# Performance work log

Hardware: AMD Instinct MI355X
Metric: run time of the kernel (lower is better)

The kernel has to match this reference:

```python
import jax, jax.numpy as jnp
import numpy as np

MIN_BW = 0.1
MAX_BW = 10.0
BW_FACTOR = 1.0
SAMPLE = 512  # min(512, B) with B >= 512


def _pairwise_dist_sq(a, b):
    # ||a_i - b_j||^2 via GEMM: [N, M], avoids [N, M, D] intermediate
    a2 = jnp.sum(a * a, axis=-1)[:, None]
    b2 = jnp.sum(b * b, axis=-1)[None, :]
    d = a2 + b2 - 2.0 * (a @ b.T)
    return jnp.maximum(d, 0.0)


def _bandwidth(x, y):
    # torch: median heuristic on first SAMPLE rows, under no_grad
    xs = jax.lax.stop_gradient(x[:SAMPLE])
    ys = jax.lax.stop_gradient(y[:SAMPLE])
    dist_sq = _pairwise_dist_sq(xs, ys)
    bw_sq = jnp.median(dist_sq.reshape(-1))
    bw = jnp.sqrt(bw_sq / 2.0) * BW_FACTOR
    return jnp.clip(bw, MIN_BW, MAX_BW)


def setup_inputs() -> dict:
    key = jax.random.key(0)
    kx, ksx, ky, ksy = jax.random.split(key, 4)
    B, D = 4096, 512
    return {
        "x": jax.random.normal(kx, (B, D), dtype=jnp.float32),
        "score_x": jax.random.normal(ksx, (B, D), dtype=jnp.float32),
        "y": jax.random.normal(ky, (B, D), dtype=jnp.float32),
        "score_y": jax.random.normal(ksy, (B, D), dtype=jnp.float32),
    }


def reference(x, score_x, y, score_y):
    D = x.shape[-1]
    h = _bandwidth(x, y)
    h2 = h * h

    dist_sq = _pairwise_dist_sq(x, y)                      # [B, B]
    k = jnp.exp(-dist_sq / (2.0 * h2))                     # [B, B]

    # term1[i,j] = k[i,j] * <score_x_i, score_y_j>
    term1 = k * (score_x @ score_y.T)

    # term2[i,j] = <x_i - y_j, score_y_j> * k[i,j] / h^2
    term2 = ((x @ score_y.T) - jnp.sum(y * score_y, axis=-1)[None, :]) * k / h2

    # term3[i,j] = ||x_i - y_j||^2 * k / h^4 - k * D / h^2
    term3 = dist_sq * k / (h2 * h2) - k * (D / h2)

    return term1 + term2 + term3
```

## Files before the change

### kernel.cpp

```cpp
#include <hip/hip_runtime.h>
#include <hip/hip_bf16.h>

typedef __attribute__((ext_vector_type(8))) short bf16x8;
typedef __attribute__((ext_vector_type(4))) float f32x4;

#define B_N 4096
#define DIM 512
#define HBINS 8192

#define OFF_PARAMS 0
#define OFF_X2     256
#define OFF_Y2     16640
#define OFF_YSY    33024
#define OFF_HIST   49408
#define OFF_TILES  98304
#define MAT_ELEMS  2097152
#define WS_NEED    (OFF_TILES + (size_t)4 * MAT_ELEMS * 2)

static __device__ __forceinline__ unsigned short f2bf_rne(float f) {
    unsigned int u = __float_as_uint(f);
    u += 0x7FFFu + ((u >> 16) & 1u);
    return (unsigned short)(u >> 16);
}
static __device__ __forceinline__ float bf2f(unsigned short h) {
    return __uint_as_float(((unsigned int)h) << 16);
}

static __device__ __forceinline__ int swz(int r, int k) {
    return r * 32 + ((((k >> 3) ^ ((r >> 1) & 3))) << 3) + (k & 7);
}


__global__ __launch_bounds__(256) void k_preAll(
    const float* __restrict__ X, const float* __restrict__ Y,
    const float* __restrict__ SY, unsigned short* __restrict__ tiles,
    float* __restrict__ x2, float* __restrict__ y2, float* __restrict__ ysy,
    unsigned int* __restrict__ hist) {
    __shared__ __align__(16) unsigned short sAB[4096];
    __shared__ unsigned int hloc[HBINS];
    __shared__ float rn[128];

    int b = blockIdx.x, t = threadIdx.x;

    if (b < 512) {
        int side = b >> 8;
        int tile = (b & 255) >> 3;
        int ky = b & 7;
        unsigned short* base0 = tiles + (size_t)side * 2 * MAT_ELEMS;
        unsigned short* base1 = base0 + MAT_ELEMS;
#pragma unroll
        for (int kt2 = 0; kt2 < 2; ++kt2) {
            int kt = ky * 2 + kt2;
            unsigned short* d0 = base0 + (size_t)(tile * 16 + kt) * 4096;
            unsigned short* d1 = base1 + (size_t)(tile * 16 + kt) * 4096;
#pragma unroll
            for (int c = 0; c < 2; ++c) {
                int v = c * 256 + t;
                int r = (v >> 6) * 16 + (v & 15);
                int k = ((v >> 4) & 3) << 3;
                const float* gp = (side ? Y : X) + (size_t)(tile * 128 + r) * DIM + kt * 32 + k;
                float4 p0 = *(const float4*)gp;
                float4 p1 = *(const float4*)(gp + 4);
                float pv[8] = {p0.x, p0.y, p0.z, p0.w, p1.x, p1.y, p1.z, p1.w};
                float s1 = 0.f, s2 = 0.f;
                bf16x8 h0;
                if (side) {
                    const float* gq = SY + (size_t)(tile * 128 + r) * DIM + kt * 32 + k;
                    float4 q0 = *(const float4*)gq;
                    float4 q1 = *(const float4*)(gq + 4);
                    float qv[8] = {q0.x, q0.y, q0.z, q0.w, q1.x, q1.y, q1.z, q1.w};
                    bf16x8 h1;
#pragma unroll
                    for (int j = 0; j < 8; ++j) {
                        s1 += pv[j] * pv[j];
                        s2 += pv[j] * qv[j];
                        h0[j] = (short)f2bf_rne(pv[j]);
                        h1[j] = (short)f2bf_rne(qv[j]);
                    }
                    *(bf16x8*)&d1[v * 8] = h1;
                } else {
#pragma unroll
                    for (int j = 0; j < 8; ++j) {
                        s1 += pv[j] * pv[j];
                        h0[j] = (short)f2bf_rne(pv[j]);
                    }
                }
                *(bf16x8*)&d0[v * 8] = h0;
                s1 += __shfl_xor(s1, 16); s1 += __shfl_xor(s1, 32);
                if (side) { s2 += __shfl_xor(s2, 16); s2 += __shfl_xor(s2, 32); }
                if ((t & 48) == 0) {
                    int row = tile * 128 + r;
                    if (side == 0) {
                        atomicAdd(&x2[row], s1);
                    } else {
                        atomicAdd(&y2[row], s1);
                        atomicAdd(&ysy[row], s2);
                    }
                }
            }
        }
    } else {
        unsigned short* sA = &sAB[0];
        unsigned short* sB = &sAB[2048];
        float* x2s = &rn[0];
        float* y2s = &rn[64];
        int hb = b - 512;
        int bi = hb >> 3, bj = hb & 7;
        for (int i = t; i < HBINS; i += 256) hloc[i] = 0;

        int lane = t & 63, w = t >> 6;
        int wm = w >> 1, wn = w & 1;
        int fr = lane & 15, fko = (lane >> 4) * 8;

        f32x4 axy[2][2];
#pragma unroll
        for (int i = 0; i < 2; ++i)
#pragma unroll
            for (int j = 0; j < 2; ++j) axy[i][j] = (f32x4)0.f;

        int r = t >> 2, k0 = (t & 3) * 8;
        const float* gx = X + (size_t)(bi * 64 + r) * DIM + k0;
        const float* gy = Y + (size_t)(bj * 64 + r) * DIM + k0;

        int ixA[2], ixB[2];
#pragma unroll
        for (int fm = 0; fm < 2; ++fm) ixA[fm] = swz(wm * 32 + fm * 16 + fr, fko);
#pragma unroll
        for (int fn = 0; fn < 2; ++fn) ixB[fn] = swz(wn * 32 + fn * 16 + fr, fko);

        float na = 0.f, nb = 0.f;
        float4 A0, A1, B0, B1;
#define LDK(kt_) do {                                                       \
            A0 = *(const float4*)(gx + (kt_) * 32);                         \
            A1 = *(const float4*)(gx + (kt_) * 32 + 4);                     \
            B0 = *(const float4*)(gy + (kt_) * 32);                         \
            B1 = *(const float4*)(gy + (kt_) * 32 + 4);                     \
        } while (0)

        LDK(0);
        for (int kt = 0; kt < 16; ++kt) {
            float av[8] = {A0.x, A0.y, A0.z, A0.w, A1.x, A1.y, A1.z, A1.w};
            float bv[8] = {B0.x, B0.y, B0.z, B0.w, B1.x, B1.y, B1.z, B1.w};
            bf16x8 ha, hb2;
#pragma unroll
            for (int j = 0; j < 8; ++j) {
                na += av[j] * av[j];
                nb += bv[j] * bv[j];
                ha[j] = (short)f2bf_rne(av[j]);
                hb2[j] = (short)f2bf_rne(bv[j]);
            }
            __syncthreads();
            *(bf16x8*)&sA[swz(r, k0)] = ha;
            *(bf16x8*)&sB[swz(r, k0)] = hb2;
            if (kt < 15) LDK(kt + 1);
            __syncthreads();

            bf16x8 aX[2];
#pragma unroll
            for (int fm = 0; fm < 2; ++fm) aX[fm] = *(const bf16x8*)&sA[ixA[fm]];
#pragma unroll
            for (int fn = 0; fn < 2; ++fn) {
                bf16x8 bY = *(const bf16x8*)&sB[ixB[fn]];
#pragma unroll
                for (int fm = 0; fm < 2; ++fm)
                    axy[fm][fn] = __builtin_amdgcn_mfma_f32_16x16x32_bf16(aX[fm], bY, axy[fm][fn], 0, 0, 0);
            }
        }
#undef LDK

        na += __shfl_xor(na, 1); na += __shfl_xor(na, 2);
        nb += __shfl_xor(nb, 1); nb += __shfl_xor(nb, 2);
        if ((t & 3) == 0) { x2s[r] = na; y2s[r] = nb; }
        __syncthreads();

        int fq = lane >> 4;
#pragma unroll
        for (int fm = 0; fm < 2; ++fm)
#pragma unroll
            for (int fn = 0; fn < 2; ++fn)
#pragma unroll
                for (int rr = 0; rr < 4; ++rr) {
                    int rl = wm * 32 + fm * 16 + fq * 4 + rr;
                    int cl = wn * 32 + fn * 16 + fr;
                    float d = fmaxf(x2s[rl] + y2s[cl] - 2.0f * axy[fm][fn][rr], 0.0f);
                    int bin = (int)(d * 4.0f);
                    if (bin > HBINS - 1) bin = HBINS - 1;
                    atomicAdd(&hloc[bin], 1u);
                }
        __syncthreads();
        for (int i = t; i < HBINS; i += 256) {
            unsigned int v = hloc[i];
            if (v) atomicAdd(&hist[i], v);
        }
    }
}

__global__ __launch_bounds__(256, 1) void k_median(
    const unsigned int* __restrict__ hist, float* __restrict__ params) {
    __shared__ unsigned int hsum[HBINS];
    __shared__ unsigned int part[256];
    __shared__ float vv[2];
    int t = threadIdx.x;
    for (int i = t; i < HBINS / 4; i += 256)
        ((uint4*)hsum)[i] = ((const uint4*)hist)[i];
    __syncthreads();
    unsigned int s = 0;
#pragma unroll 8
    for (int b = t * 32; b < t * 32 + 32; ++b) s += hsum[b];
    part[t] = s;
    __syncthreads();
    unsigned int pre = 0;
    for (int i = 0; i < 256; ++i) {
        unsigned int v = part[i];
        if (i < t) pre += v;
    }
    const unsigned int kk1 = 131072u, kk2 = 131073u;
    unsigned int hi = pre + s;
#pragma unroll
    for (int sel = 0; sel < 2; ++sel) {
        unsigned int kk = sel ? kk2 : kk1;
        if (kk > pre && kk <= hi) {
            unsigned int cc = pre;
            for (int b = 0; b < 32; ++b) {
                cc += hsum[t * 32 + b];
                if (cc >= kk) { vv[sel] = ((float)(t * 32 + b) + 0.5f) * 0.25f; break; }
            }
        }
    }
    __syncthreads();
    if (t == 0) {
        float med = 0.5f * (vv[0] + vv[1]);
        float bw = sqrtf(med * 0.5f);
        bw = fminf(fmaxf(bw, 0.1f), 10.0f);
        float h2 = bw * bw;
        params[0] = 1.0f / (2.0f * h2);
        params[1] = 1.0f / h2;
        params[2] = 1.0f / (h2 * h2);
        params[3] = (float)DIM / h2;
    }
}

__global__ __launch_bounds__(256) void k_preC(
    const float* __restrict__ X, const float* __restrict__ SX,
    const float* __restrict__ params, unsigned short* __restrict__ tiles) {
    float c1 = params[1];
    int tile = blockIdx.x, t = threadIdx.x;
    unsigned short* base1 = tiles + MAT_ELEMS;
#pragma unroll
    for (int kt2 = 0; kt2 < 2; ++kt2) {
        int kt = blockIdx.y * 2 + kt2;
        unsigned short* d1 = base1 + (size_t)(tile * 16 + kt) * 4096;
#pragma unroll
        for (int c = 0; c < 2; ++c) {
            int v = c * 256 + t;
            int r = (v >> 6) * 16 + (v & 15);
            int k = ((v >> 4) & 3) << 3;
            const float* gp = X + (size_t)(tile * 128 + r) * DIM + kt * 32 + k;
            const float* gq = SX + (size_t)(tile * 128 + r) * DIM + kt * 32 + k;
            float4 p0 = *(const float4*)gp;
            float4 p1 = *(const float4*)(gp + 4);
            float4 q0 = *(const float4*)gq;
            float4 q1 = *(const float4*)(gq + 4);
            float pv[8] = {p0.x, p0.y, p0.z, p0.w, p1.x, p1.y, p1.z, p1.w};
            float qv[8] = {q0.x, q0.y, q0.z, q0.w, q1.x, q1.y, q1.z, q1.w};
            bf16x8 h1;
#pragma unroll
            for (int j = 0; j < 8; ++j) h1[j] = (short)f2bf_rne(qv[j] + c1 * pv[j]);
            *(bf16x8*)&d1[v * 8] = h1;
        }
    }
}

#define GLD(g, l) __builtin_amdgcn_global_load_lds(                                   \
    (const __attribute__((address_space(1))) void*)(g),                               \
    (__attribute__((address_space(3))) void*)(l), 16, 0, 0)

__global__ __launch_bounds__(256, 2) void k_main(
    const unsigned short* __restrict__ tiles,
    const float* __restrict__ x2g, const float* __restrict__ y2g,
    const float* __restrict__ ysyg, const float* __restrict__ params,
    float* __restrict__ out) {
    __shared__ __align__(16) unsigned short sA[2][4096];
    __shared__ __align__(16) unsigned short sB[2][4096];
    __shared__ float x2s[128], y2s[128], ysys[128];

    int t = threadIdx.x;
    int bm = blockIdx.y, bn = blockIdx.x;
    if (t < 128) x2s[t] = x2g[bm * 128 + t];
    else { y2s[t - 128] = y2g[bn * 128 + (t - 128)]; ysys[t - 128] = ysyg[bn * 128 + (t - 128)]; }
    __syncthreads();

    int lane = t & 63, w = t >> 6;
    int wm = w >> 1, wn = w & 1;

    f32x4 axy[4][4], acb[4][4];
#pragma unroll
    for (int i = 0; i < 4; ++i)
#pragma unroll
        for (int j = 0; j < 4; ++j) { axy[i][j] = (f32x4)0.f; acb[i][j] = (f32x4)0.f; }

    const unsigned short* gaX = tiles + (size_t)(bm * 16) * 4096 + t * 8;
    const unsigned short* gbY = tiles + (size_t)2 * MAT_ELEMS + (size_t)(bn * 16) * 4096 + t * 8;
    const unsigned short* gaC = tiles + (size_t)MAT_ELEMS + (size_t)(bm * 16) * 4096
                              + (wm * 4) * 512 + lane * 8;
    const unsigned short* gbS = tiles + (size_t)3 * MAT_ELEMS + (size_t)(bn * 16) * 4096
                              + (wn * 4) * 512 + lane * 8;

#define STAGE(buf, kt_) do {                                                     \
        const unsigned short* pa_ = gaX + (size_t)(kt_) * 4096;                  \
        const unsigned short* pb_ = gbY + (size_t)(kt_) * 4096;                  \
        GLD(pa_,        &sA[buf][t * 8]);                                        \
        GLD(pa_ + 2048, &sA[buf][2048 + t * 8]);                                 \
        GLD(pb_,        &sB[buf][t * 8]);                                        \
        GLD(pb_ + 2048, &sB[buf][2048 + t * 8]);                                 \
    } while (0)

#define FRAGLD(dC, dS, kt_) do {                                                 \
        const unsigned short* pc_ = gaC + (size_t)(kt_) * 4096;                  \
        const unsigned short* ps_ = gbS + (size_t)(kt_) * 4096;                  \
        dC[0] = *(const bf16x8*)(pc_);        dS[0] = *(const bf16x8*)(ps_);     \
        dC[1] = *(const bf16x8*)(pc_ + 512);  dS[1] = *(const bf16x8*)(ps_ + 512);\
        dC[2] = *(const bf16x8*)(pc_ + 1024); dS[2] = *(const bf16x8*)(ps_ + 1024);\
        dC[3] = *(const bf16x8*)(pc_ + 1536); dS[3] = *(const bf16x8*)(ps_ + 1536);\
    } while (0)

    int ixA[4], ixB[4];
#pragma unroll
    for (int fm = 0; fm < 4; ++fm) ixA[fm] = (wm * 4 + fm) * 512 + lane * 8;
#pragma unroll
    for (int fn = 0; fn < 4; ++fn) ixB[fn] = (wn * 4 + fn) * 512 + lane * 8;

    bf16x8 fC0[4], fS0[4], fC1[4], fS1[4];

#define KSTEP(CB, CURC, CURS, NXTC, NXTS, NKT, DOPF) do {                        \
        asm volatile("s_waitcnt vmcnt(8)" ::: "memory");   \
        __builtin_amdgcn_sched_barrier(0);                                       \
        __builtin_amdgcn_s_barrier();                                            \
        __builtin_amdgcn_sched_barrier(0);                                       \
        if (DOPF) {                                                              \
            STAGE(CB ^ 1, NKT);                                                  \
            FRAGLD(NXTC, NXTS, NKT);                                             \
        }                                                                        \
        bf16x8 dX[4], dY[4];                                                     \
        dX[0] = *(const bf16x8*)&sA[CB][ixA[0]];                                 \
        dX[1] = *(const bf16x8*)&sA[CB][ixA[1]];                                 \
        dX[2] = *(const bf16x8*)&sA[CB][ixA[2]];                                 \
        dX[3] = *(const bf16x8*)&sA[CB][ixA[3]];                                 \
        dY[0] = *(const bf16x8*)&sB[CB][ixB[0]];                                 \
        dY[1] = *(const bf16x8*)&sB[CB][ixB[1]];                                 \
        dY[2] = *(const bf16x8*)&sB[CB][ixB[2]];                                 \
        dY[3] = *(const bf16x8*)&sB[CB][ixB[3]];                                 \
        __builtin_amdgcn_s_setprio(1);                                           \
        _Pragma("unroll")                                                        \
        for (int fn_ = 0; fn_ < 4; ++fn_) {                                      \
            _Pragma("unroll")                                                    \
            for (int fm_ = 0; fm_ < 4; ++fm_) {                                  \
                axy[fm_][fn_] = __builtin_amdgcn_mfma_f32_16x16x32_bf16(         \
                    dX[fm_], dY[fn_], axy[fm_][fn_], 0, 0, 0);                   \
                acb[fm_][fn_] = __builtin_amdgcn_mfma_f32_16x16x32_bf16(         \
                    CURC[fm_], CURS[fn_], acb[fm_][fn_], 0, 0, 0);               \
            }                                                                    \
        }                                                                        \
        __builtin_amdgcn_s_setprio(0);                                           \
        __builtin_amdgcn_sched_barrier(0);                                       \
    } while (0)

    STAGE(0, 0);
    FRAGLD(fC0, fS0, 0);

    for (int k2 = 0; k2 < 7; ++k2) {
        KSTEP(0, fC0, fS0, fC1, fS1, 2 * k2 + 1, 1);
        KSTEP(1, fC1, fS1, fC0, fS0, 2 * k2 + 2, 1);
    }
    KSTEP(0, fC0, fS0, fC1, fS1, 15, 1);
    KSTEP(1, fC1, fS1, fC0, fS0, 0, 0);
#undef KSTEP
#undef STAGE
#undef FRAGLD

    float c0 = params[0], c1 = params[1], c2 = params[2], c3 = params[3];
    int fr = lane & 15, fq = lane >> 4;
#pragma unroll
    for (int fm = 0; fm < 4; ++fm) {
#pragma unroll
        for (int fn = 0; fn < 4; ++fn) {
#pragma unroll
            for (int r = 0; r < 4; ++r) {
                int rl = wm * 64 + fm * 16 + fq * 4 + r;
                int cl = wn * 64 + fn * 16 + fr;
                float d = fmaxf(x2s[rl] + y2s[cl] - 2.0f * axy[fm][fn][r], 0.0f);
                float kv = __expf(-d * c0);
                out[(size_t)(bm * 128 + rl) * B_N + (bn * 128 + cl)] =
                    kv * (acb[fm][fn][r] - c1 * ysys[cl] + d * c2 - c3);
            }
        }
    }
}

__global__ void k_rowstats(const float* __restrict__ X, const float* __restrict__ Y,
                           const float* __restrict__ SY,
                           float* __restrict__ x2, float* __restrict__ y2,
                           float* __restrict__ ysy) {
    int t = threadIdx.x;
    int r = blockIdx.x * 4 + (t >> 6);
    int lane = t & 63;
    const float4* px = (const float4*)(X + (size_t)r * DIM) + lane * 2;
    const float4* py = (const float4*)(Y + (size_t)r * DIM) + lane * 2;
    const float4* ps = (const float4*)(SY + (size_t)r * DIM) + lane * 2;
    float4 a0 = px[0], a1 = px[1];
    float4 b0 = py[0], b1 = py[1];
    float4 c0 = ps[0], c1 = ps[1];
    float s1 = a0.x*a0.x + a0.y*a0.y + a0.z*a0.z + a0.w*a0.w
             + a1.x*a1.x + a1.y*a1.y + a1.z*a1.z + a1.w*a1.w;
    float s2 = b0.x*b0.x + b0.y*b0.y + b0.z*b0.z + b0.w*b0.w
             + b1.x*b1.x + b1.y*b1.y + b1.z*b1.z + b1.w*b1.w;
    float s3 = b0.x*c0.x + b0.y*c0.y + b0.z*c0.z + b0.w*c0.w
             + b1.x*c1.x + b1.y*c1.y + b1.z*c1.z + b1.w*c1.w;
#pragma unroll
    for (int o = 32; o > 0; o >>= 1) {
        s1 += __shfl_down(s1, o);
        s2 += __shfl_down(s2, o);
        s3 += __shfl_down(s3, o);
    }
    if (lane == 0) { x2[r] = s1; y2[r] = s2; ysy[r] = s3; }
}

__global__ void k_hist_fp32(const float* __restrict__ X, const float* __restrict__ Y,
                            const float* __restrict__ x2, const float* __restrict__ y2,
                            unsigned int* __restrict__ hist) {
    __shared__ float xs[32][68];
    __shared__ float ys[32][68];
    __shared__ unsigned int hloc[HBINS];
    int t = threadIdx.x;
    for (int i = t; i < HBINS; i += 256) hloc[i] = 0;
    int i0 = blockIdx.y * 32, j0 = blockIdx.x * 32;
    float a00 = 0.f, a01 = 0.f, a10 = 0.f, a11 = 0.f;
    int ti = (t >> 4) * 2, tj = (t & 15) * 2;
    for (int c = 0; c < 8; ++c) {
        __syncthreads();
        int rr = t >> 3, cc = (t & 7) * 8;
        const float* gx = X + (size_t)(i0 + rr) * DIM + c * 64 + cc;
        *(float4*)&xs[rr][cc] = *(const float4*)gx;
        *(float4*)&xs[rr][cc + 4] = *(const float4*)(gx + 4);
        const float* gy = Y + (size_t)(j0 + rr) * DIM + c * 64 + cc;
        *(float4*)&ys[rr][cc] = *(const float4*)gy;
        *(float4*)&ys[rr][cc + 4] = *(const float4*)(gy + 4);
        __syncthreads();
        for (int kk = 0; kk < 64; ++kk) {
            float a0 = xs[ti][kk], a1 = xs[ti + 1][kk];
            float b0 = ys[tj][kk], b1 = ys[tj + 1][kk];
            a00 += a0 * b0; a01 += a0 * b1; a10 += a1 * b0; a11 += a1 * b1;
        }
    }
    float s[2][2] = {{a00, a01}, {a10, a11}};
#pragma unroll
    for (int ii = 0; ii < 2; ++ii)
#pragma unroll
        for (int jj = 0; jj < 2; ++jj) {
            float d = fmaxf(x2[i0 + ti + ii] + y2[j0 + tj + jj] - 2.f * s[ii][jj], 0.f);
            int bin = (int)(d * 4.0f);
            if (bin > HBINS - 1) bin = HBINS - 1;
            atomicAdd(&hloc[bin], 1u);
        }
    __syncthreads();
    for (int i = t; i < HBINS; i += 256) {
        unsigned int v = hloc[i];
        if (v) atomicAdd(&hist[i], v);
    }
}

static __device__ __forceinline__ void store_hi(unsigned short* tile, int r, int k0,
                                                float4 v0, float4 v1) {
    bf16x8 h;
    h[0] = (short)f2bf_rne(v0.x); h[1] = (short)f2bf_rne(v0.y);
    h[2] = (short)f2bf_rne(v0.z); h[3] = (short)f2bf_rne(v0.w);
    h[4] = (short)f2bf_rne(v1.x); h[5] = (short)f2bf_rne(v1.y);
    h[6] = (short)f2bf_rne(v1.z); h[7] = (short)f2bf_rne(v1.w);
    *(bf16x8*)&tile[swz(r, k0)] = h;
}
static __device__ __forceinline__ void store_hilo(unsigned short* th, unsigned short* tl,
                                                  int r, int k0, float4 v0, float4 v1) {
    float f[8] = {v0.x, v0.y, v0.z, v0.w, v1.x, v1.y, v1.z, v1.w};
    bf16x8 h, l;
#pragma unroll
    for (int j = 0; j < 8; ++j) {
        unsigned short hh = f2bf_rne(f[j]);
        h[j] = (short)hh;
        l[j] = (short)f2bf_rne(f[j] - bf2f(hh));
    }
    *(bf16x8*)&th[swz(r, k0)] = h;
    *(bf16x8*)&tl[swz(r, k0)] = l;
}

__global__ __launch_bounds__(256, 2) void k_main_fb(
    const float* __restrict__ X, const float* __restrict__ SX,
    const float* __restrict__ Y, const float* __restrict__ SY,
    const float* __restrict__ x2g, const float* __restrict__ y2g,
    const float* __restrict__ ysyg, const float* __restrict__ params,
    float* __restrict__ out) {
    __shared__ __align__(16) unsigned short tX[4096];
    __shared__ __align__(16) unsigned short tSXH[4096];
    __shared__ __align__(16) unsigned short tSXL[4096];
    __shared__ __align__(16) unsigned short tY[2048];
    __shared__ __align__(16) unsigned short tSYH[2048];
    __shared__ __align__(16) unsigned short tSYL[2048];
    __shared__ float x2s[128];
    __shared__ float y2s[64];
    __shared__ float ysys[64];

    int t = threadIdx.x;
    int bm = blockIdx.y, bn = blockIdx.x;
    if (t < 128) x2s[t] = x2g[bm * 128 + t];
    else if (t < 192) y2s[t - 128] = y2g[bn * 64 + (t - 128)];
    else ysys[t - 192] = ysyg[bn * 64 + (t - 192)];

    int lane = t & 63, w = t >> 6, wm = w >> 1, wn = w & 1;
    f32x4 axy[4][2], ass[4][2], axsy[4][2];
#pragma unroll
    for (int i = 0; i < 4; ++i)
#pragma unroll
        for (int j = 0; j < 2; ++j) {
            axy[i][j] = (f32x4)0.f; ass[i][j] = (f32x4)0.f; axsy[i][j] = (f32x4)0.f;
        }

    for (int kt = 0; kt < DIM / 32; ++kt) {
        int kb = kt * 32;
#pragma unroll
        for (int h = 0; h < 2; ++h) {
            int s = t + h * 256;
            int r = s >> 2, k0 = (s & 3) * 8;
            const float* gx = X + (size_t)(bm * 128 + r) * DIM + kb + k0;
            store_hi(tX, r, k0, *(const float4*)gx, *(const float4*)(gx + 4));
            const float* gs = SX + (size_t)(bm * 128 + r) * DIM + kb + k0;
            store_hilo(tSXH, tSXL, r, k0, *(const float4*)gs, *(const float4*)(gs + 4));
        }
        {
            int r = t >> 2, k0 = (t & 3) * 8;
            const float* gy = Y + (size_t)(bn * 64 + r) * DIM + kb + k0;
            store_hi(tY, r, k0, *(const float4*)gy, *(const float4*)(gy + 4));
            const float* gq = SY + (size_t)(bn * 64 + r) * DIM + kb + k0;
            store_hilo(tSYH, tSYL, r, k0, *(const float4*)gq, *(const float4*)(gq + 4));
        }
        __syncthreads();

        int fr = lane & 15, fk = (lane >> 4) * 8;
        bf16x8 aX[4], aSH[4], aSL[4];
#pragma unroll
        for (int fm = 0; fm < 4; ++fm) {
            int ix = swz(wm * 64 + fm * 16 + fr, fk);
            aX[fm] = *(const bf16x8*)&tX[ix];
            aSH[fm] = *(const bf16x8*)&tSXH[ix];
            aSL[fm] = *(const bf16x8*)&tSXL[ix];
        }
#pragma unroll
        for (int fn = 0; fn < 2; ++fn) {
            int iy = swz(wn * 32 + fn * 16 + fr, fk);
            bf16x8 bY = *(const bf16x8*)&tY[iy];
            bf16x8 bH = *(const bf16x8*)&tSYH[iy];
            bf16x8 bL = *(const bf16x8*)&tSYL[iy];
#pragma unroll
            for (int fm = 0; fm < 4; ++fm) {
                axy[fm][fn] = __builtin_amdgcn_mfma_f32_16x16x32_bf16(aX[fm], bY, axy[fm][fn], 0, 0, 0);
                ass[fm][fn] = __builtin_amdgcn_mfma_f32_16x16x32_bf16(aSH[fm], bH, ass[fm][fn], 0, 0, 0);
                ass[fm][fn] = __builtin_amdgcn_mfma_f32_16x16x32_bf16(aSH[fm], bL, ass[fm][fn], 0, 0, 0);
                ass[fm][fn] = __builtin_amdgcn_mfma_f32_16x16x32_bf16(aSL[fm], bH, ass[fm][fn], 0, 0, 0);
                axsy[fm][fn] = __builtin_amdgcn_mfma_f32_16x16x32_bf16(aX[fm], bH, axsy[fm][fn], 0, 0, 0);
            }
        }
        __syncthreads();
    }

    float c0 = params[0], c1 = params[1], c2 = params[2], c3 = params[3];
    int fr = lane & 15, fq = lane >> 4;
#pragma unroll
    for (int fm = 0; fm < 4; ++fm)
#pragma unroll
        for (int fn = 0; fn < 2; ++fn)
#pragma unroll
            for (int r = 0; r < 4; ++r) {
                int rl = wm * 64 + fm * 16 + fq * 4 + r;
                int cl = wn * 32 + fn * 16 + fr;
                float d = fmaxf(x2s[rl] + y2s[cl] - 2.0f * axy[fm][fn][r], 0.0f);
                float kv = __expf(-d * c0);
                out[(size_t)(bm * 128 + rl) * B_N + (bn * 64 + cl)] =
                    kv * ass[fm][fn][r] + (axsy[fm][fn][r] - ysys[cl]) * (kv * c1)
                    + d * kv * c2 - kv * c3;
            }
}

extern "C" void kernel_launch(void* const* d_in, const int* in_sizes, int n_in,
                              void* d_out, int out_size, void* d_ws, size_t ws_size,
                              hipStream_t stream) {
    const float* x  = (const float*)d_in[0];
    const float* sx = (const float*)d_in[1];
    const float* y  = (const float*)d_in[2];
    const float* sy = (const float*)d_in[3];
    float* out = (float*)d_out;
    char* ws = (char*)d_ws;
    float* params = (float*)(ws + OFF_PARAMS);
    float* x2 = (float*)(ws + OFF_X2);
    float* y2 = (float*)(ws + OFF_Y2);
    float* ysy = (float*)(ws + OFF_YSY);
    unsigned int* hist = (unsigned int*)(ws + OFF_HIST);
    unsigned short* tiles = (unsigned short*)(ws + OFF_TILES);

    if (ws_size >= WS_NEED) {
        hipMemsetAsync(ws + OFF_X2, 0, 3 * 16384 + HBINS * 4, stream);
        k_preAll<<<576, 256, 0, stream>>>(x, y, sy, tiles, x2, y2, ysy, hist);
        k_median<<<1, 256, 0, stream>>>(hist, params);
        k_preC<<<dim3(32, 8), 256, 0, stream>>>(x, sx, params, tiles);
        k_main<<<dim3(32, 32), dim3(256), 0, stream>>>(tiles, x2, y2, ysy, params, out);
    } else {
        hipMemsetAsync(hist, 0, HBINS * 4, stream);
        k_rowstats<<<B_N / 4, 256, 0, stream>>>(x, y, sy, x2, y2, ysy);
        k_hist_fp32<<<dim3(16, 16), dim3(256), 0, stream>>>(x, y, x2, y2, hist);
        k_median<<<1, 256, 0, stream>>>(hist, params);
        k_main_fb<<<dim3(64, 32), dim3(256), 0, stream>>>(x, sx, y, sy, x2, y2, ysy, params, out);
    }
}
```

Before: 82.28 us.

## Fuse median into preC and deepen main GEMM LDS pipeline to three stages

Every k_preC block now reads the global histogram and computes the median and bandwidth itself. This removes the separate single-block k_median launch and its serialization gap, at the cost of redundant histogram scans in each block. k_main moves from a double-buffered to a triple-buffered LDS ring with a deeper prefetch distance and adjusted vmcnt waits, so global loads are issued further ahead of use. The extra LDS (48KB tiles) may reduce occupancy below the two blocks per CU the launch bounds request.

```diff
diff --git a/kernel.cpp b/kernel.cpp
--- a/kernel.cpp
+++ b/kernel.cpp
@@ -28,6 +28,34 @@
 
 static __device__ __forceinline__ int swz(int r, int k) {
     return r * 32 + ((((k >> 3) ^ ((r >> 1) & 3))) << 3) + (k & 7);
+}
+
+static __device__ __forceinline__ void median_from_lds(
+    unsigned int* hsum, unsigned int* part, float* vv, int t) {
+    unsigned int s = 0;
+#pragma unroll 8
+    for (int b = t * 32; b < t * 32 + 32; ++b) s += hsum[b];
+    part[t] = s;
+    __syncthreads();
+    unsigned int pre = 0;
+    for (int i = 0; i < 256; ++i) {
+        unsigned int v = part[i];
+        if (i < t) pre += v;
+    }
+    const unsigned int kk1 = 131072u, kk2 = 131073u;
+    unsigned int hi = pre + s;
+#pragma unroll
+    for (int sel = 0; sel < 2; ++sel) {
+        unsigned int kk = sel ? kk2 : kk1;
+        if (kk > pre && kk <= hi) {
+            unsigned int cc = pre;
+            for (int b = 0; b < 32; ++b) {
+                cc += hsum[t * 32 + b];
+                if (cc >= kk) { vv[sel] = ((float)(t * 32 + b) + 0.5f) * 0.25f; break; }
+            }
+        }
+    }
+    __syncthreads();
 }
 
 
@@ -195,8 +223,10 @@
     }
 }
 
-__global__ __launch_bounds__(256, 1) void k_median(
-    const unsigned int* __restrict__ hist, float* __restrict__ params) {
+__global__ __launch_bounds__(256) void k_preC(
+    const float* __restrict__ X, const float* __restrict__ SX,
+    const unsigned int* __restrict__ hist, float* __restrict__ params,
+    unsigned short* __restrict__ tiles) {
     __shared__ unsigned int hsum[HBINS];
     __shared__ unsigned int part[256];
     __shared__ float vv[2];
@@ -204,47 +234,19 @@
     for (int i = t; i < HBINS / 4; i += 256)
         ((uint4*)hsum)[i] = ((const uint4*)hist)[i];
     __syncthreads();
-    unsigned int s = 0;
-#pragma unroll 8
-    for (int b = t * 32; b < t * 32 + 32; ++b) s += hsum[b];
-    part[t] = s;
-    __syncthreads();
-    unsigned int pre = 0;
-    for (int i = 0; i < 256; ++i) {
-        unsigned int v = part[i];
-        if (i < t) pre += v;
-    }
-    const unsigned int kk1 = 131072u, kk2 = 131073u;
-    unsigned int hi = pre + s;
-#pragma unroll
-    for (int sel = 0; sel < 2; ++sel) {
-        unsigned int kk = sel ? kk2 : kk1;
-        if (kk > pre && kk <= hi) {
-            unsigned int cc = pre;
-            for (int b = 0; b < 32; ++b) {
-                cc += hsum[t * 32 + b];
-                if (cc >= kk) { vv[sel] = ((float)(t * 32 + b) + 0.5f) * 0.25f; break; }
-            }
-        }
-    }
-    __syncthreads();
-    if (t == 0) {
-        float med = 0.5f * (vv[0] + vv[1]);
-        float bw = sqrtf(med * 0.5f);
-        bw = fminf(fmaxf(bw, 0.1f), 10.0f);
-        float h2 = bw * bw;
+    median_from_lds(hsum, part, vv, t);
+    float med = 0.5f * (vv[0] + vv[1]);
+    float bw = fminf(fmaxf(sqrtf(med * 0.5f), 0.1f), 10.0f);
+    float h2 = bw * bw;
+    float c1 = 1.0f / h2;
+    if (blockIdx.x == 0 && blockIdx.y == 0 && t == 0) {
         params[0] = 1.0f / (2.0f * h2);
-        params[1] = 1.0f / h2;
+        params[1] = c1;
         params[2] = 1.0f / (h2 * h2);
         params[3] = (float)DIM / h2;
     }
-}
-
-__global__ __launch_bounds__(256) void k_preC(
-    const float* __restrict__ X, const float* __restrict__ SX,
-    const float* __restrict__ params, unsigned short* __restrict__ tiles) {
-    float c1 = params[1];
-    int tile = blockIdx.x, t = threadIdx.x;
+
+    int tile = blockIdx.x;
     unsigned short* base1 = tiles + MAT_ELEMS;
 #pragma unroll
     for (int kt2 = 0; kt2 < 2; ++kt2) {
@@ -280,8 +282,8 @@
     const float* __restrict__ x2g, const float* __restrict__ y2g,
     const float* __restrict__ ysyg, const float* __restrict__ params,
     float* __restrict__ out) {
-    __shared__ __align__(16) unsigned short sA[2][4096];
-    __shared__ __align__(16) unsigned short sB[2][4096];
+    __shared__ __align__(16) unsigned short sA[3][4096];
+    __shared__ __align__(16) unsigned short sB[3][4096];
     __shared__ float x2s[128], y2s[128], ysys[128];
 
     int t = threadIdx.x;
@@ -332,15 +334,13 @@
 
     bf16x8 fC0[4], fS0[4], fC1[4], fS1[4];
 
-#define KSTEP(CB, CURC, CURS, NXTC, NXTS, NKT, DOPF) do {                        \
-        asm volatile("s_waitcnt vmcnt(8)" ::: "memory");   \
+#define KSTEP(CB, CURC, CURS, NXTC, NXTS, SKT, FKT, MODE, WAITN) do {            \
+        asm volatile("s_waitcnt vmcnt(" #WAITN ")" ::: "memory");                \
         __builtin_amdgcn_sched_barrier(0);                                       \
         __builtin_amdgcn_s_barrier();                                            \
         __builtin_amdgcn_sched_barrier(0);                                       \
-        if (DOPF) {                                                              \
-            STAGE(CB ^ 1, NKT);                                                  \
-            FRAGLD(NXTC, NXTS, NKT);                                             \
-        }                                                                        \
+        if (MODE >= 1) FRAGLD(NXTC, NXTS, FKT);                                  \
+        if (MODE == 2) STAGE(((CB) + 2) % 3, SKT);                               \
         bf16x8 dX[4], dY[4];                                                     \
         dX[0] = *(const bf16x8*)&sA[CB][ixA[0]];                                 \
         dX[1] = *(const bf16x8*)&sA[CB][ixA[1]];                                 \
@@ -367,13 +367,21 @@
 
     STAGE(0, 0);
     FRAGLD(fC0, fS0, 0);
-
-    for (int k2 = 0; k2 < 7; ++k2) {
-        KSTEP(0, fC0, fS0, fC1, fS1, 2 * k2 + 1, 1);
-        KSTEP(1, fC1, fS1, fC0, fS0, 2 * k2 + 2, 1);
-    }
-    KSTEP(0, fC0, fS0, fC1, fS1, 15, 1);
-    KSTEP(1, fC1, fS1, fC0, fS0, 0, 0);
+    STAGE(1, 1);
+
+    for (int k6 = 0; k6 < 2; ++k6) {
+        int kt = k6 * 6;
+        KSTEP(0, fC0, fS0, fC1, fS1, kt + 2, kt + 1, 2, 12);
+        KSTEP(1, fC1, fS1, fC0, fS0, kt + 3, kt + 2, 2, 12);
+        KSTEP(2, fC0, fS0, fC1, fS1, kt + 4, kt + 3, 2, 12);
+        KSTEP(0, fC1, fS1, fC0, fS0, kt + 5, kt + 4, 2, 12);
+        KSTEP(1, fC0, fS0, fC1, fS1, kt + 6, kt + 5, 2, 12);
+        KSTEP(2, fC1, fS1, fC0, fS0, kt + 7, kt + 6, 2, 12);
+    }
+    KSTEP(0, fC0, fS0, fC1, fS1, 14, 13, 2, 12);
+    KSTEP(1, fC1, fS1, fC0, fS0, 15, 14, 2, 12);
+    KSTEP(2, fC0, fS0, fC1, fS1, 0, 15, 1, 12);
+    KSTEP(0, fC1, fS1, fC0, fS0, 0, 0, 0, 8);
 #undef KSTEP
 #undef STAGE
 #undef FRAGLD
@@ -469,6 +477,27 @@
     }
 }
 
+__global__ __launch_bounds__(256, 1) void k_median(
+    const unsigned int* __restrict__ hist, float* __restrict__ params) {
+    __shared__ unsigned int hsum[HBINS];
+    __shared__ unsigned int part[256];
+    __shared__ float vv[2];
+    int t = threadIdx.x;
+    for (int i = t; i < HBINS / 4; i += 256)
+        ((uint4*)hsum)[i] = ((const uint4*)hist)[i];
+    __syncthreads();
+    median_from_lds(hsum, part, vv, t);
+    if (t == 0) {
+        float med = 0.5f * (vv[0] + vv[1]);
+        float bw = fminf(fmaxf(sqrtf(med * 0.5f), 0.1f), 10.0f);
+        float h2 = bw * bw;
+        params[0] = 1.0f / (2.0f * h2);
+        params[1] = 1.0f / h2;
+        params[2] = 1.0f / (h2 * h2);
+        params[3] = (float)DIM / h2;
+    }
+}
+
 static __device__ __forceinline__ void store_hi(unsigned short* tile, int r, int k0,
                                                 float4 v0, float4 v1) {
     bf16x8 h;
@@ -607,8 +636,7 @@
     if (ws_size >= WS_NEED) {
         hipMemsetAsync(ws + OFF_X2, 0, 3 * 16384 + HBINS * 4, stream);
         k_preAll<<<576, 256, 0, stream>>>(x, y, sy, tiles, x2, y2, ysy, hist);
-        k_median<<<1, 256, 0, stream>>>(hist, params);
-        k_preC<<<dim3(32, 8), 256, 0, stream>>>(x, sx, params, tiles);
+        k_preC<<<dim3(32, 8), 256, 0, stream>>>(x, sx, hist, params, tiles);
         k_main<<<dim3(32, 32), dim3(256), 0, stream>>>(tiles, x2, y2, ysy, params, out);
     } else {
         hipMemsetAsync(hist, 0, HBINS * 4, stream);
```

After: 83.64 us. No clear change (+1.6%).
